# Kernel optimization log

Measured on AMD Instinct MI355X. Metric: run time of the kernel, lower is better.

The kernel has to match this reference:

```python
import jax, jax.numpy as jnp
import numpy as np

B = 4096
OBS_DIM = 1024
E_OUT = 512
H1 = 2048
H2 = 2048


def setup_inputs() -> dict:
    key = jax.random.key(0)
    ks = jax.random.split(key, 12)
    def kaiming(k, shape, fan_in):
        return jax.random.normal(k, shape, dtype=jnp.float32) * np.float32(np.sqrt(2.0 / fan_in))
    obs = jax.random.normal(ks[0], (B, OBS_DIM), dtype=jnp.float32)
    # lineare: Linear(obs_dim, e_outputs), torch weight shape [out, in]
    We = kaiming(ks[1], (E_OUT, OBS_DIM), OBS_DIM)
    be = jax.random.normal(ks[2], (E_OUT,), dtype=jnp.float32) * 0.01
    # obs_dim attention heads, each Linear(e_outputs, 2), stacked
    attn_W = kaiming(ks[3], (OBS_DIM, E_OUT, 2), E_OUT)
    attn_b = jax.random.normal(ks[4], (OBS_DIM, 2), dtype=jnp.float32) * 0.01
    # v_net: Linear(obs_dim,H1)+tanh, Linear(H1,H2)+[dropout(eval:no-op)]+tanh, Linear(H2,1)
    W1 = kaiming(ks[5], (H1, OBS_DIM), OBS_DIM)
    b1 = jnp.zeros((H1,), dtype=jnp.float32)
    W2 = kaiming(ks[6], (H2, H1), H1)
    b2 = jnp.zeros((H2,), dtype=jnp.float32)
    W3 = kaiming(ks[7], (1, H2), H2)
    b3 = jnp.zeros((1,), dtype=jnp.float32)
    return {"obs": obs, "We": We, "be": be, "attn_W": attn_W, "attn_b": attn_b,
            "W1": W1, "b1": b1, "W2": W2, "b2": b2, "W3": W3, "b3": b3}


def reference(obs, We, be, attn_W, attn_b, W1, b1, W2, b2, W3, b3):
    # e = tanh(lineare(obs)) : [B, E_OUT]
    e = jnp.tanh(obs @ We.T + be)
    # all obs_dim attention heads batched into one contraction: [B, OBS_DIM, 2]
    logits = jnp.einsum('be,oec->boc', e, attn_W) + attn_b
    # softmax over the 2 logits, keep prob of class 1 -> Attention [B, OBS_DIM]
    attention = jax.nn.softmax(logits, axis=-1)[..., 1]
    state_attention = obs * attention
    # v_net (eval mode: dropout is identity)
    h = jnp.tanh(state_attention @ W1.T + b1)
    h = jnp.tanh(h @ W2.T + b2)
    v = jnp.squeeze(h @ W3.T + b3, -1)  # [B]
    return (v, attention)
```

## Files before the change

### kernel.cpp

```cpp
#include <hip/hip_runtime.h>
#include <hip/hip_bf16.h>

typedef unsigned short u16;
typedef u16 u16x4 __attribute__((ext_vector_type(4)));
typedef u16 u16x8 __attribute__((ext_vector_type(8)));
typedef __bf16 bf16x8 __attribute__((ext_vector_type(8)));
typedef float f32x4 __attribute__((ext_vector_type(4)));

__device__ __forceinline__ u16 f2bf(float f) {
  unsigned u = __float_as_uint(f);
  u += 0x7FFFu + ((u >> 16) & 1u);
  return (u16)(u >> 16);
}
__device__ __forceinline__ float bf2f(u16 h) {
  return __uint_as_float(((unsigned)h) << 16);
}
__device__ __forceinline__ float tanh_fast(float x) {
  float t = __expf(2.0f * x);
  return 1.0f - 2.0f / (t + 1.0f);
}
__device__ __forceinline__ float sigmoid_fast(float x) {
  return 1.0f / (1.0f + __expf(-x));
}

__device__ __forceinline__ void async16(const void* g, void* lds) {
  __builtin_amdgcn_global_load_lds(
      (const __attribute__((address_space(1))) unsigned int*)g,
      (__attribute__((address_space(3))) unsigned int*)lds,
      16, 0, 0);
}

__device__ __forceinline__ void cvt4(const float* __restrict__ s, u16* __restrict__ d, int q) {
  float4 v = ((const float4*)s)[q];
  u16x4 o = { f2bf(v.x), f2bf(v.y), f2bf(v.z), f2bf(v.w) };
  ((u16x4*)d)[q] = o;
}

__global__ __launch_bounds__(256)
void prep_kernel(const float* __restrict__ obs, const float* __restrict__ We,
                 const float* __restrict__ W1, const float* __restrict__ W2,
                 const float* __restrict__ aW, const float* __restrict__ ab,
                 u16* __restrict__ obs_b, u16* __restrict__ We_b,
                 u16* __restrict__ W1_b, u16* __restrict__ W2_b,
                 u16* __restrict__ Wd, float* __restrict__ bd) {
  int q = blockIdx.x * 256 + threadIdx.x;
  if (q < 1048576) { cvt4(obs, obs_b, q); return; }
  q -= 1048576;
  if (q < 131072) { cvt4(We, We_b, q); return; }
  q -= 131072;
  if (q < 524288) { cvt4(W1, W1_b, q); return; }
  q -= 524288;
  if (q < 1048576) { cvt4(W2, W2_b, q); return; }
  q -= 1048576;
  if (q < 131072) {
    int i0 = q * 4;
    int o = i0 >> 9, e0 = i0 & 511;
    const float* p = aW + (size_t)o * 1024 + e0 * 2;
    float4 v0 = *(const float4*)p;
    float4 v1 = *(const float4*)(p + 4);
    u16x4 od = { f2bf(v0.y - v0.x), f2bf(v0.w - v0.z),
                 f2bf(v1.y - v1.x), f2bf(v1.w - v1.z) };
    *(u16x4*)(Wd + i0) = od;
    if (q < 256) {
      float4 a0 = *(const float4*)(ab + q * 8);
      float4 a1 = *(const float4*)(ab + q * 8 + 4);
      float4 ob = { a0.y - a0.x, a0.w - a0.z, a1.y - a1.x, a1.w - a1.z };
      *(float4*)(bd + q * 4) = ob;
    }
  }
}

template <int BM, int BN, int EP>
__global__ __launch_bounds__(256)
void gemm_bt(const u16* __restrict__ A, const u16* __restrict__ Bt,
             int M, int N, int K,
             const float* __restrict__ bias,
             u16* __restrict__ outb,
             float* __restrict__ outf,
             const float* __restrict__ obs,
             u16* __restrict__ sa) {
  constexpr int MI = BM / 32;
  constexpr int NJ = BN / 32;
  constexpr int CA = BM / 16;
  constexpr int CHUNKS = (BM + BN) / 16;
  constexpr int CPW = CHUNKS / 4;

  __shared__ __align__(16) u16 As[2][BM * 32];
  __shared__ __align__(16) u16 Bs[2][BN * 32];

  const int tid = threadIdx.x;
  const int lane = tid & 63;
  const int wave = tid >> 6;
  const int bm = blockIdx.x;
  const int bn = blockIdx.y;

  const u16* gsrc[CPW];
  u16* ld0[CPW];
  u16* ld1[CPW];
#pragma unroll
  for (int q = 0; q < CPW; ++q) {
    const int c = wave * CPW + q;
    if (c < CA) {
      const int r = c * 16;
      gsrc[q] = A + (size_t)(bm * BM + r + (lane >> 2)) * K + (lane & 3) * 8;
      ld0[q] = &As[0][r * 32];
      ld1[q] = &As[1][r * 32];
    } else {
      const int r = (c - CA) * 16;
      gsrc[q] = Bt + (size_t)(bn * BN + r + (lane >> 2)) * K + (lane & 3) * 8;
      ld0[q] = &Bs[0][r * 32];
      ld1[q] = &Bs[1][r * 32];
    }
  }

  const int wm = (wave >> 1) * (BM / 2);
  const int wn = (wave & 1) * (BN / 2);
  const int fr = lane & 15;
  const int koff = (lane >> 4) * 8;

  const int T = K >> 5;

#pragma unroll
  for (int q = 0; q < CPW; ++q) async16(gsrc[q], ld0[q]);
#pragma unroll
  for (int q = 0; q < CPW; ++q) gsrc[q] += 32;

  f32x4 acc[MI][NJ];
#pragma unroll
  for (int i = 0; i < MI; ++i)
#pragma unroll
    for (int j = 0; j < NJ; ++j)
      acc[i][j] = (f32x4){0.f, 0.f, 0.f, 0.f};

  for (int k = 0; k < T; ++k) {
    __syncthreads();
    if (k + 1 < T) {
      const int nxt = (k + 1) & 1;
#pragma unroll
      for (int q = 0; q < CPW; ++q) async16(gsrc[q], nxt ? ld1[q] : ld0[q]);
#pragma unroll
      for (int q = 0; q < CPW; ++q) gsrc[q] += 32;
    }
    const u16* Ar = &As[k & 1][0];
    const u16* Br = &Bs[k & 1][0];

    bf16x8 a[MI], b[NJ];
#pragma unroll
    for (int i = 0; i < MI; ++i)
      a[i] = *(const bf16x8*)(Ar + (wm + i * 16 + fr) * 32 + koff);
#pragma unroll
    for (int j = 0; j < NJ; ++j)
      b[j] = *(const bf16x8*)(Br + (wn + j * 16 + fr) * 32 + koff);
#pragma unroll
    for (int i = 0; i < MI; ++i)
#pragma unroll
      for (int j = 0; j < NJ; ++j)
        acc[i][j] = __builtin_amdgcn_mfma_f32_16x16x32_bf16(a[i], b[j], acc[i][j], 0, 0, 0);
  }

#pragma unroll
  for (int j = 0; j < NJ; ++j) {
    const int col = bn * BN + wn + j * 16 + fr;
    const float bv = bias[col];
#pragma unroll
    for (int i = 0; i < MI; ++i) {
#pragma unroll
      for (int r = 0; r < 4; ++r) {
        const int row = bm * BM + wm + i * 16 + (lane >> 4) * 4 + r;
        const float x = acc[i][j][r] + bv;
        const size_t idx = (size_t)row * N + col;
        if (EP == 0) {
          outb[idx] = f2bf(tanh_fast(x));
        } else {
          const float att = sigmoid_fast(x);
          outf[idx] = att;
          sa[idx] = f2bf(obs[idx] * att);
        }
      }
    }
  }
}

__global__ __launch_bounds__(256)
void gemv_v(const u16* __restrict__ h2, const float* __restrict__ W3,
            const float* __restrict__ b3, float* __restrict__ out) {
  int g = blockIdx.x * 256 + threadIdx.x;
  int row = g >> 6;
  int lane = g & 63;
  const u16* rp = h2 + (size_t)row * 2048;
  float sum = 0.f;
#pragma unroll
  for (int p = 0; p < 4; ++p) {
    int base = p * 512 + lane * 8;
    u16x8 hv = *(const u16x8*)(rp + base);
    float4 w0 = *(const float4*)(W3 + base);
    float4 w1 = *(const float4*)(W3 + base + 4);
    sum += bf2f(hv[0]) * w0.x + bf2f(hv[1]) * w0.y + bf2f(hv[2]) * w0.z + bf2f(hv[3]) * w0.w;
    sum += bf2f(hv[4]) * w1.x + bf2f(hv[5]) * w1.y + bf2f(hv[6]) * w1.z + bf2f(hv[7]) * w1.w;
  }
#pragma unroll
  for (int off = 32; off > 0; off >>= 1) sum += __shfl_down(sum, off);
  if (lane == 0) out[row] = sum + b3[0];
}

extern "C" void kernel_launch(void* const* d_in, const int* in_sizes, int n_in,
                              void* d_out, int out_size, void* d_ws, size_t ws_size,
                              hipStream_t stream) {
  const float* obs   = (const float*)d_in[0];
  const float* We    = (const float*)d_in[1];
  const float* be    = (const float*)d_in[2];
  const float* attnW = (const float*)d_in[3];
  const float* attnb = (const float*)d_in[4];
  const float* W1    = (const float*)d_in[5];
  const float* b1    = (const float*)d_in[6];
  const float* W2    = (const float*)d_in[7];
  const float* b2    = (const float*)d_in[8];
  const float* W3    = (const float*)d_in[9];
  const float* b3    = (const float*)d_in[10];
  float* out = (float*)d_out;

  char* ws = (char*)d_ws;
  u16*   We_b  = (u16*)(ws + 0x00000000);
  u16*   Wd_b  = (u16*)(ws + 0x00100000);
  u16*   W1_b  = (u16*)(ws + 0x00200000);
  u16*   W2_b  = (u16*)(ws + 0x00600000);
  float* bd    = (float*)(ws + 0x00E00000);
  u16*   obs_b = (u16*)(ws + 0x00E01000);
  u16*   e_b   = (u16*)(ws + 0x01601000);
  u16*   sa_b  = (u16*)(ws + 0x01A01000);
  u16*   h1_b  = (u16*)(ws + 0x02201000);
  u16*   h2_b  = (u16*)(ws + 0x03201000);

  prep_kernel<<<11264, 256, 0, stream>>>(obs, We, W1, W2, attnW, attnb,
                                         obs_b, We_b, W1_b, W2_b, Wd_b, bd);

  gemm_bt<64, 64, 0><<<dim3(64, 8), 256, 0, stream>>>(obs_b, We_b, 4096, 512, 1024, be, e_b, nullptr, nullptr, nullptr);
  gemm_bt<64, 64, 1><<<dim3(64, 16), 256, 0, stream>>>(e_b, Wd_b, 4096, 1024, 512, bd, nullptr, out + 4096, obs, sa_b);
  gemm_bt<128, 64, 0><<<dim3(32, 32), 256, 0, stream>>>(sa_b, W1_b, 4096, 2048, 1024, b1, h1_b, nullptr, nullptr, nullptr);
  gemm_bt<128, 64, 0><<<dim3(32, 32), 256, 0, stream>>>(h1_b, W2_b, 4096, 2048, 2048, b2, h2_b, nullptr, nullptr, nullptr);
  gemv_v<<<1024, 256, 0, stream>>>(h2_b, W3, b3, out);
}
```

Baseline: 218.5 us.

## Fuse fp32-to-bf16 conversion into GEMM loads and drop the prep kernel

```diff
diff --git a/kernel.cpp b/kernel.cpp
--- a/kernel.cpp
+++ b/kernel.cpp
@@ -2,7 +2,6 @@
 #include <hip/hip_bf16.h>
 
 typedef unsigned short u16;
-typedef u16 u16x4 __attribute__((ext_vector_type(4)));
 typedef u16 u16x8 __attribute__((ext_vector_type(8)));
 typedef __bf16 bf16x8 __attribute__((ext_vector_type(8)));
 typedef float f32x4 __attribute__((ext_vector_type(4)));
@@ -23,107 +22,110 @@
   return 1.0f / (1.0f + __expf(-x));
 }
 
-__device__ __forceinline__ void async16(const void* g, void* lds) {
-  __builtin_amdgcn_global_load_lds(
-      (const __attribute__((address_space(1))) unsigned int*)g,
-      (__attribute__((address_space(3))) unsigned int*)lds,
-      16, 0, 0);
-}
-
-__device__ __forceinline__ void cvt4(const float* __restrict__ s, u16* __restrict__ d, int q) {
-  float4 v = ((const float4*)s)[q];
-  u16x4 o = { f2bf(v.x), f2bf(v.y), f2bf(v.z), f2bf(v.w) };
-  ((u16x4*)d)[q] = o;
-}
-
+__device__ __forceinline__ u16x8 pack8(float4 a, float4 b) {
+  u16x8 o;
+  o[0] = f2bf(a.x); o[1] = f2bf(a.y); o[2] = f2bf(a.z); o[3] = f2bf(a.w);
+  o[4] = f2bf(b.x); o[5] = f2bf(b.y); o[6] = f2bf(b.z); o[7] = f2bf(b.w);
+  return o;
+}
+__device__ __forceinline__ u16x8 pack8d(const float4* v) {
+  u16x8 o;
+  o[0] = f2bf(v[0].y - v[0].x); o[1] = f2bf(v[0].w - v[0].z);
+  o[2] = f2bf(v[1].y - v[1].x); o[3] = f2bf(v[1].w - v[1].z);
+  o[4] = f2bf(v[2].y - v[2].x); o[5] = f2bf(v[2].w - v[2].z);
+  o[6] = f2bf(v[3].y - v[3].x); o[7] = f2bf(v[3].w - v[3].z);
+  return o;
+}
+
+template <int BM, int BN, int AMODE, int BMODE, int EP>
 __global__ __launch_bounds__(256)
-void prep_kernel(const float* __restrict__ obs, const float* __restrict__ We,
-                 const float* __restrict__ W1, const float* __restrict__ W2,
-                 const float* __restrict__ aW, const float* __restrict__ ab,
-                 u16* __restrict__ obs_b, u16* __restrict__ We_b,
-                 u16* __restrict__ W1_b, u16* __restrict__ W2_b,
-                 u16* __restrict__ Wd, float* __restrict__ bd) {
-  int q = blockIdx.x * 256 + threadIdx.x;
-  if (q < 1048576) { cvt4(obs, obs_b, q); return; }
-  q -= 1048576;
-  if (q < 131072) { cvt4(We, We_b, q); return; }
-  q -= 131072;
-  if (q < 524288) { cvt4(W1, W1_b, q); return; }
-  q -= 524288;
-  if (q < 1048576) { cvt4(W2, W2_b, q); return; }
-  q -= 1048576;
-  if (q < 131072) {
-    int i0 = q * 4;
-    int o = i0 >> 9, e0 = i0 & 511;
-    const float* p = aW + (size_t)o * 1024 + e0 * 2;
-    float4 v0 = *(const float4*)p;
-    float4 v1 = *(const float4*)(p + 4);
-    u16x4 od = { f2bf(v0.y - v0.x), f2bf(v0.w - v0.z),
-                 f2bf(v1.y - v1.x), f2bf(v1.w - v1.z) };
-    *(u16x4*)(Wd + i0) = od;
-    if (q < 256) {
-      float4 a0 = *(const float4*)(ab + q * 8);
-      float4 a1 = *(const float4*)(ab + q * 8 + 4);
-      float4 ob = { a0.y - a0.x, a0.w - a0.z, a1.y - a1.x, a1.w - a1.z };
-      *(float4*)(bd + q * 4) = ob;
-    }
-  }
-}
-
-template <int BM, int BN, int EP>
-__global__ __launch_bounds__(256)
-void gemm_bt(const u16* __restrict__ A, const u16* __restrict__ Bt,
-             int M, int N, int K,
-             const float* __restrict__ bias,
-             u16* __restrict__ outb,
-             float* __restrict__ outf,
-             const float* __restrict__ obs,
-             u16* __restrict__ sa) {
+void gemm_f(const void* __restrict__ Avp, const void* __restrict__ Bvp,
+            int N, int K,
+            const float* __restrict__ bias,
+            u16* __restrict__ outb, float* __restrict__ outf,
+            const float* __restrict__ obs, u16* __restrict__ sa) {
+  constexpr int CA = BM / 64;
+  constexpr int CB = BN / 64;
   constexpr int MI = BM / 32;
   constexpr int NJ = BN / 32;
-  constexpr int CA = BM / 16;
-  constexpr int CHUNKS = (BM + BN) / 16;
-  constexpr int CPW = CHUNKS / 4;
-
-  __shared__ __align__(16) u16 As[2][BM * 32];
-  __shared__ __align__(16) u16 Bs[2][BN * 32];
+
+  __shared__ __align__(16) u16 As[BM * 32];
+  __shared__ __align__(16) u16 Bs[BN * 32];
 
   const int tid = threadIdx.x;
   const int lane = tid & 63;
   const int wave = tid >> 6;
-  const int bm = blockIdx.x;
-  const int bn = blockIdx.y;
-
-  const u16* gsrc[CPW];
-  u16* ld0[CPW];
-  u16* ld1[CPW];
-#pragma unroll
-  for (int q = 0; q < CPW; ++q) {
-    const int c = wave * CPW + q;
-    if (c < CA) {
-      const int r = c * 16;
-      gsrc[q] = A + (size_t)(bm * BM + r + (lane >> 2)) * K + (lane & 3) * 8;
-      ld0[q] = &As[0][r * 32];
-      ld1[q] = &As[1][r * 32];
-    } else {
-      const int r = (c - CA) * 16;
-      gsrc[q] = Bt + (size_t)(bn * BN + r + (lane >> 2)) * K + (lane & 3) * 8;
-      ld0[q] = &Bs[0][r * 32];
-      ld1[q] = &Bs[1][r * 32];
-    }
-  }
+  const int bm = blockIdx.x, bn = blockIdx.y;
+
+  const int sr = tid >> 2;
+  const int c0 = (tid & 3) * 8;
+
+  const u16* gA16[CA]; const float* gA32[CA];
+  const u16* gB16[CB]; const float* gB32[CB];
+#pragma unroll
+  for (int q = 0; q < CA; ++q) {
+    const size_t row = bm * BM + sr + q * 64;
+    if constexpr (AMODE == 0) gA16[q] = (const u16*)Avp + row * K + c0;
+    else                      gA32[q] = (const float*)Avp + row * K + c0;
+  }
+#pragma unroll
+  for (int q = 0; q < CB; ++q) {
+    const size_t row = bn * BN + sr + q * 64;
+    if constexpr (BMODE == 0)      gB16[q] = (const u16*)Bvp + row * K + c0;
+    else if constexpr (BMODE == 1) gB32[q] = (const float*)Bvp + row * K + c0;
+    else                           gB32[q] = (const float*)Bvp + row * (size_t)(2 * K) + c0 * 2;
+  }
+
+  u16x8 pa16[CA]; float4 pa32[CA][2];
+  u16x8 pb16[CB]; float4 pb32[CB][4];
+
+  auto fetch = [&]() {
+#pragma unroll
+    for (int q = 0; q < CA; ++q) {
+      if constexpr (AMODE == 0) { pa16[q] = *(const u16x8*)gA16[q]; gA16[q] += 32; }
+      else {
+        pa32[q][0] = *(const float4*)gA32[q];
+        pa32[q][1] = *(const float4*)(gA32[q] + 4);
+        gA32[q] += 32;
+      }
+    }
+#pragma unroll
+    for (int q = 0; q < CB; ++q) {
+      if constexpr (BMODE == 0) { pb16[q] = *(const u16x8*)gB16[q]; gB16[q] += 32; }
+      else if constexpr (BMODE == 1) {
+        pb32[q][0] = *(const float4*)gB32[q];
+        pb32[q][1] = *(const float4*)(gB32[q] + 4);
+        gB32[q] += 32;
+      } else {
+#pragma unroll
+        for (int r = 0; r < 4; ++r) pb32[q][r] = *(const float4*)(gB32[q] + 4 * r);
+        gB32[q] += 64;
+      }
+    }
+  };
+
+  auto stage = [&]() {
+#pragma unroll
+    for (int q = 0; q < CA; ++q) {
+      u16x8* w = (u16x8*)(As + (sr + q * 64) * 32 + c0);
+      if constexpr (AMODE == 0) *w = pa16[q];
+      else                      *w = pack8(pa32[q][0], pa32[q][1]);
+    }
+#pragma unroll
+    for (int q = 0; q < CB; ++q) {
+      u16x8* w = (u16x8*)(Bs + (sr + q * 64) * 32 + c0);
+      if constexpr (BMODE == 0)      *w = pb16[q];
+      else if constexpr (BMODE == 1) *w = pack8(pb32[q][0], pb32[q][1]);
+      else                           *w = pack8d(pb32[q]);
+    }
+  };
 
   const int wm = (wave >> 1) * (BM / 2);
   const int wn = (wave & 1) * (BN / 2);
   const int fr = lane & 15;
   const int koff = (lane >> 4) * 8;
 
-  const int T = K >> 5;
-
-#pragma unroll
-  for (int q = 0; q < CPW; ++q) async16(gsrc[q], ld0[q]);
-#pragma unroll
-  for (int q = 0; q < CPW; ++q) gsrc[q] += 32;
+  fetch();
 
   f32x4 acc[MI][NJ];
 #pragma unroll
@@ -132,25 +134,20 @@
     for (int j = 0; j < NJ; ++j)
       acc[i][j] = (f32x4){0.f, 0.f, 0.f, 0.f};
 
+  const int T = K >> 5;
   for (int k = 0; k < T; ++k) {
     __syncthreads();
-    if (k + 1 < T) {
-      const int nxt = (k + 1) & 1;
-#pragma unroll
-      for (int q = 0; q < CPW; ++q) async16(gsrc[q], nxt ? ld1[q] : ld0[q]);
-#pragma unroll
-      for (int q = 0; q < CPW; ++q) gsrc[q] += 32;
-    }
-    const u16* Ar = &As[k & 1][0];
-    const u16* Br = &Bs[k & 1][0];
+    stage();
+    __syncthreads();
+    if (k + 1 < T) fetch();
 
     bf16x8 a[MI], b[NJ];
 #pragma unroll
     for (int i = 0; i < MI; ++i)
-      a[i] = *(const bf16x8*)(Ar + (wm + i * 16 + fr) * 32 + koff);
+      a[i] = *(const bf16x8*)(As + (wm + i * 16 + fr) * 32 + koff);
 #pragma unroll
     for (int j = 0; j < NJ; ++j)
-      b[j] = *(const bf16x8*)(Br + (wn + j * 16 + fr) * 32 + koff);
+      b[j] = *(const bf16x8*)(Bs + (wn + j * 16 + fr) * 32 + koff);
 #pragma unroll
     for (int i = 0; i < MI; ++i)
 #pragma unroll
@@ -161,7 +158,9 @@
 #pragma unroll
   for (int j = 0; j < NJ; ++j) {
     const int col = bn * BN + wn + j * 16 + fr;
-    const float bv = bias[col];
+    float bv;
+    if constexpr (EP == 0) bv = bias[col];
+    else                   bv = bias[2 * col + 1] - bias[2 * col];
 #pragma unroll
     for (int i = 0; i < MI; ++i) {
 #pragma unroll
@@ -169,7 +168,7 @@
         const int row = bm * BM + wm + i * 16 + (lane >> 4) * 4 + r;
         const float x = acc[i][j][r] + bv;
         const size_t idx = (size_t)row * N + col;
-        if (EP == 0) {
+        if constexpr (EP == 0) {
           outb[idx] = f2bf(tanh_fast(x));
         } else {
           const float att = sigmoid_fast(x);
@@ -220,23 +219,18 @@
   float* out = (float*)d_out;
 
   char* ws = (char*)d_ws;
-  u16*   We_b  = (u16*)(ws + 0x00000000);
-  u16*   Wd_b  = (u16*)(ws + 0x00100000);
-  u16*   W1_b  = (u16*)(ws + 0x00200000);
-  u16*   W2_b  = (u16*)(ws + 0x00600000);
-  float* bd    = (float*)(ws + 0x00E00000);
-  u16*   obs_b = (u16*)(ws + 0x00E01000);
-  u16*   e_b   = (u16*)(ws + 0x01601000);
-  u16*   sa_b  = (u16*)(ws + 0x01A01000);
-  u16*   h1_b  = (u16*)(ws + 0x02201000);
-  u16*   h2_b  = (u16*)(ws + 0x03201000);
-
-  prep_kernel<<<11264, 256, 0, stream>>>(obs, We, W1, W2, attnW, attnb,
-                                         obs_b, We_b, W1_b, W2_b, Wd_b, bd);
-
-  gemm_bt<64, 64, 0><<<dim3(64, 8), 256, 0, stream>>>(obs_b, We_b, 4096, 512, 1024, be, e_b, nullptr, nullptr, nullptr);
-  gemm_bt<64, 64, 1><<<dim3(64, 16), 256, 0, stream>>>(e_b, Wd_b, 4096, 1024, 512, bd, nullptr, out + 4096, obs, sa_b);
-  gemm_bt<128, 64, 0><<<dim3(32, 32), 256, 0, stream>>>(sa_b, W1_b, 4096, 2048, 1024, b1, h1_b, nullptr, nullptr, nullptr);
-  gemm_bt<128, 64, 0><<<dim3(32, 32), 256, 0, stream>>>(h1_b, W2_b, 4096, 2048, 2048, b2, h2_b, nullptr, nullptr, nullptr);
+  u16* e_b  = (u16*)(ws + 0x0000000);
+  u16* sa_b = (u16*)(ws + 0x0400000);
+  u16* h1_b = (u16*)(ws + 0x0C00000);
+  u16* h2_b = (u16*)(ws + 0x1C00000);
+
+  gemm_f<64, 64, 1, 1, 0><<<dim3(64, 8), 256, 0, stream>>>(
+      obs, We, 512, 1024, be, e_b, nullptr, nullptr, nullptr);
+  gemm_f<128, 64, 0, 2, 1><<<dim3(32, 16), 256, 0, stream>>>(
+      e_b, attnW, 1024, 512, attnb, nullptr, out + 4096, obs, sa_b);
+  gemm_f<128, 128, 0, 1, 0><<<dim3(32, 16), 256, 0, stream>>>(
+      sa_b, W1, 2048, 1024, b1, h1_b, nullptr, nullptr, nullptr);
+  gemm_f<128, 128, 0, 1, 0><<<dim3(32, 16), 256, 0, stream>>>(
+      h1_b, W2, 2048, 2048, b2, h2_b, nullptr, nullptr, nullptr);
   gemv_v<<<1024, 256, 0, stream>>>(h2_b, W3, b3, out);
 }
```

After: 254.3 us. 16.4% more time.

## Fuse final GEMV into last GEMM epilogue and switch to register-staged loads

Applied to the files above, without the earlier changes.

```diff
diff --git a/kernel.cpp b/kernel.cpp
--- a/kernel.cpp
+++ b/kernel.cpp
@@ -21,13 +21,6 @@
 }
 __device__ __forceinline__ float sigmoid_fast(float x) {
   return 1.0f / (1.0f + __expf(-x));
-}
-
-__device__ __forceinline__ void async16(const void* g, void* lds) {
-  __builtin_amdgcn_global_load_lds(
-      (const __attribute__((address_space(1))) unsigned int*)g,
-      (__attribute__((address_space(3))) unsigned int*)lds,
-      16, 0, 0);
 }
 
 __device__ __forceinline__ void cvt4(const float* __restrict__ s, u16* __restrict__ d, int q) {
@@ -73,58 +66,48 @@
 template <int BM, int BN, int EP>
 __global__ __launch_bounds__(256)
 void gemm_bt(const u16* __restrict__ A, const u16* __restrict__ Bt,
-             int M, int N, int K,
+             int N, int K,
              const float* __restrict__ bias,
-             u16* __restrict__ outb,
-             float* __restrict__ outf,
-             const float* __restrict__ obs,
-             u16* __restrict__ sa) {
+             u16* __restrict__ outb, float* __restrict__ outf,
+             const float* __restrict__ obs, u16* __restrict__ sa,
+             const float* __restrict__ W3, const float* __restrict__ b3,
+             float* __restrict__ vout) {
+  constexpr int CA = BM / 64;
+  constexpr int CB = BN / 64;
   constexpr int MI = BM / 32;
   constexpr int NJ = BN / 32;
-  constexpr int CA = BM / 16;
-  constexpr int CHUNKS = (BM + BN) / 16;
-  constexpr int CPW = CHUNKS / 4;
-
-  __shared__ __align__(16) u16 As[2][BM * 32];
-  __shared__ __align__(16) u16 Bs[2][BN * 32];
+
+  __shared__ __align__(16) u16 As[BM * 32];
+  __shared__ __align__(16) u16 Bs[BN * 32];
 
   const int tid = threadIdx.x;
   const int lane = tid & 63;
   const int wave = tid >> 6;
-  const int bm = blockIdx.x;
-  const int bn = blockIdx.y;
-
-  const u16* gsrc[CPW];
-  u16* ld0[CPW];
-  u16* ld1[CPW];
-#pragma unroll
-  for (int q = 0; q < CPW; ++q) {
-    const int c = wave * CPW + q;
-    if (c < CA) {
-      const int r = c * 16;
-      gsrc[q] = A + (size_t)(bm * BM + r + (lane >> 2)) * K + (lane & 3) * 8;
-      ld0[q] = &As[0][r * 32];
-      ld1[q] = &As[1][r * 32];
-    } else {
-      const int r = (c - CA) * 16;
-      gsrc[q] = Bt + (size_t)(bn * BN + r + (lane >> 2)) * K + (lane & 3) * 8;
-      ld0[q] = &Bs[0][r * 32];
-      ld1[q] = &Bs[1][r * 32];
-    }
-  }
+  const int bm = blockIdx.x, bn = blockIdx.y;
+
+  const int sr = tid >> 2;
+  const int c0 = (tid & 3) * 8;
+
+  const u16* gA[CA];
+  const u16* gB[CB];
+#pragma unroll
+  for (int q = 0; q < CA; ++q)
+    gA[q] = A + (size_t)(bm * BM + sr + q * 64) * K + c0;
+#pragma unroll
+  for (int q = 0; q < CB; ++q)
+    gB[q] = Bt + (size_t)(bn * BN + sr + q * 64) * K + c0;
+
+  u16x8 pa[CA], pb[CB];
+#pragma unroll
+  for (int q = 0; q < CA; ++q) { pa[q] = *(const u16x8*)gA[q]; gA[q] += 32; }
+#pragma unroll
+  for (int q = 0; q < CB; ++q) { pb[q] = *(const u16x8*)gB[q]; gB[q] += 32; }
 
   const int wm = (wave >> 1) * (BM / 2);
   const int wn = (wave & 1) * (BN / 2);
   const int fr = lane & 15;
   const int koff = (lane >> 4) * 8;
 
-  const int T = K >> 5;
-
-#pragma unroll
-  for (int q = 0; q < CPW; ++q) async16(gsrc[q], ld0[q]);
-#pragma unroll
-  for (int q = 0; q < CPW; ++q) gsrc[q] += 32;
-
   f32x4 acc[MI][NJ];
 #pragma unroll
   for (int i = 0; i < MI; ++i)
@@ -132,25 +115,29 @@
     for (int j = 0; j < NJ; ++j)
       acc[i][j] = (f32x4){0.f, 0.f, 0.f, 0.f};
 
+  const int T = K >> 5;
   for (int k = 0; k < T; ++k) {
     __syncthreads();
+#pragma unroll
+    for (int q = 0; q < CA; ++q) *(u16x8*)(As + (sr + q * 64) * 32 + c0) = pa[q];
+#pragma unroll
+    for (int q = 0; q < CB; ++q) *(u16x8*)(Bs + (sr + q * 64) * 32 + c0) = pb[q];
+    __syncthreads();
+
     if (k + 1 < T) {
-      const int nxt = (k + 1) & 1;
-#pragma unroll
-      for (int q = 0; q < CPW; ++q) async16(gsrc[q], nxt ? ld1[q] : ld0[q]);
-#pragma unroll
-      for (int q = 0; q < CPW; ++q) gsrc[q] += 32;
-    }
-    const u16* Ar = &As[k & 1][0];
-    const u16* Br = &Bs[k & 1][0];
+#pragma unroll
+      for (int q = 0; q < CA; ++q) { pa[q] = *(const u16x8*)gA[q]; gA[q] += 32; }
+#pragma unroll
+      for (int q = 0; q < CB; ++q) { pb[q] = *(const u16x8*)gB[q]; gB[q] += 32; }
+    }
 
     bf16x8 a[MI], b[NJ];
 #pragma unroll
     for (int i = 0; i < MI; ++i)
-      a[i] = *(const bf16x8*)(Ar + (wm + i * 16 + fr) * 32 + koff);
+      a[i] = *(const bf16x8*)(As + (wm + i * 16 + fr) * 32 + koff);
 #pragma unroll
     for (int j = 0; j < NJ; ++j)
-      b[j] = *(const bf16x8*)(Br + (wn + j * 16 + fr) * 32 + koff);
+      b[j] = *(const bf16x8*)(Bs + (wn + j * 16 + fr) * 32 + koff);
 #pragma unroll
     for (int i = 0; i < MI; ++i)
 #pragma unroll
@@ -158,49 +145,62 @@
         acc[i][j] = __builtin_amdgcn_mfma_f32_16x16x32_bf16(a[i], b[j], acc[i][j], 0, 0, 0);
   }
 
-#pragma unroll
-  for (int j = 0; j < NJ; ++j) {
-    const int col = bn * BN + wn + j * 16 + fr;
-    const float bv = bias[col];
-#pragma unroll
-    for (int i = 0; i < MI; ++i) {
+  if constexpr (EP == 2) {
+    float vpart[MI][4];
+#pragma unroll
+    for (int i = 0; i < MI; ++i)
+#pragma unroll
+      for (int r = 0; r < 4; ++r) vpart[i][r] = 0.f;
+#pragma unroll
+    for (int j = 0; j < NJ; ++j) {
+      const int col = bn * BN + wn + j * 16 + fr;
+      const float bv = bias[col];
+      const float w3 = W3[col];
+#pragma unroll
+      for (int i = 0; i < MI; ++i)
+#pragma unroll
+        for (int r = 0; r < 4; ++r)
+          vpart[i][r] += tanh_fast(acc[i][j][r] + bv) * w3;
+    }
+    const bool lead = (fr == 0);
+    const bool addb = (bn == 0) && ((wave & 1) == 0);
+#pragma unroll
+    for (int i = 0; i < MI; ++i)
 #pragma unroll
       for (int r = 0; r < 4; ++r) {
-        const int row = bm * BM + wm + i * 16 + (lane >> 4) * 4 + r;
-        const float x = acc[i][j][r] + bv;
-        const size_t idx = (size_t)row * N + col;
-        if (EP == 0) {
-          outb[idx] = f2bf(tanh_fast(x));
-        } else {
-          const float att = sigmoid_fast(x);
-          outf[idx] = att;
-          sa[idx] = f2bf(obs[idx] * att);
+        float p = vpart[i][r];
+        p += __shfl_xor(p, 8);
+        p += __shfl_xor(p, 4);
+        p += __shfl_xor(p, 2);
+        p += __shfl_xor(p, 1);
+        if (lead) {
+          const int row = bm * BM + wm + i * 16 + (lane >> 4) * 4 + r;
+          atomicAdd(vout + row, addb ? p + b3[0] : p);
         }
       }
+  } else {
+#pragma unroll
+    for (int j = 0; j < NJ; ++j) {
+      const int col = bn * BN + wn + j * 16 + fr;
+      const float bv = bias[col];
+#pragma unroll
+      for (int i = 0; i < MI; ++i) {
+#pragma unroll
+        for (int r = 0; r < 4; ++r) {
+          const int row = bm * BM + wm + i * 16 + (lane >> 4) * 4 + r;
+          const float x = acc[i][j][r] + bv;
+          const size_t idx = (size_t)row * N + col;
+          if constexpr (EP == 0) {
+            outb[idx] = f2bf(tanh_fast(x));
+          } else {
+            const float att = sigmoid_fast(x);
+            outf[idx] = att;
+            sa[idx] = f2bf(obs[idx] * att);
+          }
+        }
+      }
     }
   }
-}
-
-__global__ __launch_bounds__(256)
-void gemv_v(const u16* __restrict__ h2, const float* __restrict__ W3,
-            const float* __restrict__ b3, float* __restrict__ out) {
-  int g = blockIdx.x * 256 + threadIdx.x;
-  int row = g >> 6;
-  int lane = g & 63;
-  const u16* rp = h2 + (size_t)row * 2048;
-  float sum = 0.f;
-#pragma unroll
-  for (int p = 0; p < 4; ++p) {
-    int base = p * 512 + lane * 8;
-    u16x8 hv = *(const u16x8*)(rp + base);
-    float4 w0 = *(const float4*)(W3 + base);
-    float4 w1 = *(const float4*)(W3 + base + 4);
-    sum += bf2f(hv[0]) * w0.x + bf2f(hv[1]) * w0.y + bf2f(hv[2]) * w0.z + bf2f(hv[3]) * w0.w;
-    sum += bf2f(hv[4]) * w1.x + bf2f(hv[5]) * w1.y + bf2f(hv[6]) * w1.z + bf2f(hv[7]) * w1.w;
-  }
-#pragma unroll
-  for (int off = 32; off > 0; off >>= 1) sum += __shfl_down(sum, off);
-  if (lane == 0) out[row] = sum + b3[0];
 }
 
 extern "C" void kernel_launch(void* const* d_in, const int* in_sizes, int n_in,
@@ -229,14 +229,18 @@
   u16*   e_b   = (u16*)(ws + 0x01601000);
   u16*   sa_b  = (u16*)(ws + 0x01A01000);
   u16*   h1_b  = (u16*)(ws + 0x02201000);
-  u16*   h2_b  = (u16*)(ws + 0x03201000);
+
+  hipMemsetAsync(out, 0, 4096 * sizeof(float), stream);
 
   prep_kernel<<<11264, 256, 0, stream>>>(obs, We, W1, W2, attnW, attnb,
                                          obs_b, We_b, W1_b, W2_b, Wd_b, bd);
 
-  gemm_bt<64, 64, 0><<<dim3(64, 8), 256, 0, stream>>>(obs_b, We_b, 4096, 512, 1024, be, e_b, nullptr, nullptr, nullptr);
-  gemm_bt<64, 64, 1><<<dim3(64, 16), 256, 0, stream>>>(e_b, Wd_b, 4096, 1024, 512, bd, nullptr, out + 4096, obs, sa_b);
-  gemm_bt<128, 64, 0><<<dim3(32, 32), 256, 0, stream>>>(sa_b, W1_b, 4096, 2048, 1024, b1, h1_b, nullptr, nullptr, nullptr);
-  gemm_bt<128, 64, 0><<<dim3(32, 32), 256, 0, stream>>>(h1_b, W2_b, 4096, 2048, 2048, b2, h2_b, nullptr, nullptr, nullptr);
-  gemv_v<<<1024, 256, 0, stream>>>(h2_b, W3, b3, out);
-}
+  gemm_bt<128, 64, 0><<<dim3(32, 8), 256, 0, stream>>>(
+      obs_b, We_b, 512, 1024, be, e_b, nullptr, nullptr, nullptr, nullptr, nullptr, nullptr);
+  gemm_bt<128, 64, 1><<<dim3(32, 16), 256, 0, stream>>>(
+      e_b, Wd_b, 1024, 512, bd, nullptr, out + 4096, obs, sa_b, nullptr, nullptr, nullptr);
+  gemm_bt<128, 128, 0><<<dim3(32, 16), 256, 0, stream>>>(
+      sa_b, W1_b, 2048, 1024, b1, h1_b, nullptr, nullptr, nullptr, nullptr, nullptr, nullptr);
+  gemm_bt<128, 128, 2><<<dim3(32, 16), 256, 0, stream>>>(
+      h1_b, W2_b, 2048, 2048, b2, nullptr, nullptr, nullptr, nullptr, W3, b3, out);
+}
```

After: 217.1 us. Within noise of the previous version (-0.7%).
